# Optimization experiments

Hardware: AMD Instinct MI355X
Metric: run time of the kernel (lower is better)

The kernel has to match this reference:

```python
import jax, jax.numpy as jnp
import numpy as np

N = 50000
E = 800000
D = 128


def setup_inputs() -> dict:
    key = jax.random.key(0)
    ks = jax.random.split(key, 6)
    x = jax.random.normal(ks[0], (N, D), dtype=jnp.float32)
    edge_index = jax.random.randint(ks[1], (2, E), 0, N, dtype=jnp.int32)
    scale = 1.0 / np.sqrt(D)
    Ws = jax.random.uniform(ks[2], (D, D), jnp.float32, -scale, scale)
    bs = jax.random.uniform(ks[3], (D,), jnp.float32, -scale, scale)
    Wn = jax.random.uniform(ks[4], (D, D), jnp.float32, -scale, scale)
    bn = jax.random.uniform(ks[5], (D,), jnp.float32, -scale, scale)
    return {"x": x, "edge_index": edge_index, "Ws": Ws, "bs": bs, "Wn": Wn, "bn": bn}


def reference(x, edge_index, Ws, bs, Wn, bn):
    # x: [N, D]; edge_index: [2, E] with rows (src, dst)
    src = edge_index[0]
    dst = edge_index[1]
    n = x.shape[0]
    # scatter-sum of gathered source features onto destinations
    agg = jax.ops.segment_sum(x[src], dst, num_segments=n)  # [N, D]
    deg = jax.ops.segment_sum(jnp.ones(dst.shape, x.dtype), dst, num_segments=n)  # [N]
    neigh = agg / jnp.clip(deg, 1.0)[:, None]  # mean aggregation, clamp deg>=1
    # torch Linear: y = x @ W.T + b
    return jax.nn.relu(x @ Ws.T + bs + neigh @ Wn.T + bn)
```

## Files before the change

### kernel.cpp

```cpp
#include <hip/hip_runtime.h>

#define D 128
#define CAP 64

typedef short bf16x8 __attribute__((ext_vector_type(8)));
typedef float f32x4 __attribute__((ext_vector_type(4)));

__device__ __forceinline__ unsigned f2bf(float f) {
    unsigned u = __builtin_bit_cast(unsigned, f);
    return (u + 0x7FFFu + ((u >> 16) & 1u)) >> 16;
}
__device__ __forceinline__ float bflo(unsigned u) {
    return __builtin_bit_cast(float, u << 16);
}
__device__ __forceinline__ float bfhi(unsigned u) {
    return __builtin_bit_cast(float, u & 0xFFFF0000u);
}

__global__ __launch_bounds__(256)
void sage_prep(const float* __restrict__ x,
               const float* __restrict__ Ws,
               const float* __restrict__ Wn,
               const int* __restrict__ ei,
               unsigned short* __restrict__ xb,
               unsigned short* __restrict__ Wsb,
               unsigned short* __restrict__ Wnb,
               unsigned short* __restrict__ srcs,
               int* __restrict__ cnt,
               int nD4, int DD4, int convBlocks, int E)
{
    const int tid = threadIdx.x;
    if ((int)blockIdx.x < convBlocks) {
        int i4 = blockIdx.x * 256 + tid;
        const float* src; unsigned short* dst; int off;
        if (i4 < nD4)                { src = x;  dst = xb;  off = i4; }
        else if (i4 < nD4 + DD4)     { src = Ws; dst = Wsb; off = i4 - nD4; }
        else if (i4 < nD4 + 2 * DD4) { src = Wn; dst = Wnb; off = i4 - nD4 - DD4; }
        else return;
        float4 v = reinterpret_cast<const float4*>(src)[off];
        ushort4 o;
        o.x = (unsigned short)f2bf(v.x);
        o.y = (unsigned short)f2bf(v.y);
        o.z = (unsigned short)f2bf(v.z);
        o.w = (unsigned short)f2bf(v.w);
        reinterpret_cast<ushort4*>(dst)[off] = o;
    } else {
        int e = (blockIdx.x - convBlocks) * 256 + tid;
        if (e < E) {
            int src = ei[e];
            int dst = ei[E + e];
            int pos = atomicAdd(&cnt[dst], 1);
            if (pos < CAP) srcs[dst * CAP + pos] = (unsigned short)src;
        }
    }
}

__global__ void sage_gather(const unsigned* __restrict__ xb32,
                            const unsigned short* __restrict__ srcs,
                            const int* __restrict__ cnt,
                            unsigned* __restrict__ nb32, int n)
{
    int wid = __builtin_amdgcn_readfirstlane(
        blockIdx.x * (blockDim.x >> 6) + (threadIdx.x >> 6));
    if (wid >= n) return;
    int lane = threadIdx.x & 63;
    int c = cnt[wid];
    if (c > CAP) c = CAP;
    const unsigned short* b = srcs + (size_t)wid * CAP;
    float ax = 0.0f, ay = 0.0f;
    int i = 0;
    for (; i + 3 < c; i += 4) {
        int s0 = b[i + 0];
        int s1 = b[i + 1];
        int s2 = b[i + 2];
        int s3 = b[i + 3];
        unsigned u0 = xb32[(size_t)s0 * 64 + lane];
        unsigned u1 = xb32[(size_t)s1 * 64 + lane];
        unsigned u2 = xb32[(size_t)s2 * 64 + lane];
        unsigned u3 = xb32[(size_t)s3 * 64 + lane];
        ax += (bflo(u0) + bflo(u1)) + (bflo(u2) + bflo(u3));
        ay += (bfhi(u0) + bfhi(u1)) + (bfhi(u2) + bfhi(u3));
    }
    for (; i < c; ++i) {
        unsigned u0 = xb32[(size_t)b[i] * 64 + lane];
        ax += bflo(u0);
        ay += bfhi(u0);
    }
    float inv = 1.0f / fmaxf((float)c, 1.0f);
    nb32[(size_t)wid * 64 + lane] = f2bf(ax * inv) | (f2bf(ay * inv) << 16);
}

__global__ __launch_bounds__(256)
void sage_mfma(const unsigned short* __restrict__ xb,
               const unsigned short* __restrict__ nb,
               const unsigned short* __restrict__ Wsb,
               const unsigned short* __restrict__ Wnb,
               const float* __restrict__ bs,
               const float* __restrict__ bn,
               float* __restrict__ out, int n, int ntiles)
{
    int wave = (blockIdx.x * blockDim.x + threadIdx.x) >> 6;
    if (wave >= ntiles) return;
    int lane = threadIdx.x & 63;
    int r0 = wave * 16;
    int arow = r0 + (lane & 15);
    if (arow >= n) arow = n - 1;
    int kq = (lane >> 4) * 8;

    const unsigned short* xrow = xb + (size_t)arow * D + kq;
    const unsigned short* nrow = nb + (size_t)arow * D + kq;
    bf16x8 axf[4], anf[4];
#pragma unroll
    for (int ks = 0; ks < 4; ++ks) {
        axf[ks] = *reinterpret_cast<const bf16x8*>(xrow + ks * 32);
        anf[ks] = *reinterpret_cast<const bf16x8*>(nrow + ks * 32);
    }

    const int jl = lane & 15;
    const int outrow0 = r0 + (lane >> 4) * 4;
#pragma unroll
    for (int c = 0; c < 8; ++c) {
        int j = c * 16 + jl;
        const unsigned short* wsrow = Wsb + (size_t)j * D + kq;
        const unsigned short* wnrow = Wnb + (size_t)j * D + kq;
        f32x4 acc = {0.f, 0.f, 0.f, 0.f};
#pragma unroll
        for (int ks = 0; ks < 4; ++ks) {
            bf16x8 bsf = *reinterpret_cast<const bf16x8*>(wsrow + ks * 32);
            bf16x8 bnf = *reinterpret_cast<const bf16x8*>(wnrow + ks * 32);
            acc = __builtin_amdgcn_mfma_f32_16x16x32_bf16(axf[ks], bsf, acc, 0, 0, 0);
            acc = __builtin_amdgcn_mfma_f32_16x16x32_bf16(anf[ks], bnf, acc, 0, 0, 0);
        }
        float bias = bs[j] + bn[j];
#pragma unroll
        for (int r = 0; r < 4; ++r) {
            int row = outrow0 + r;
            if (row < n) {
                float v = acc[r] + bias;
                out[(size_t)row * D + j] = v > 0.f ? v : 0.f;
            }
        }
    }
}

extern "C" void kernel_launch(void* const* d_in, const int* in_sizes, int n_in,
                              void* d_out, int out_size, void* d_ws, size_t ws_size,
                              hipStream_t stream)
{
    const float* x  = (const float*)d_in[0];
    const int*   ei = (const int*)d_in[1];
    const float* Ws = (const float*)d_in[2];
    const float* bs = (const float*)d_in[3];
    const float* Wn = (const float*)d_in[4];
    const float* bn = (const float*)d_in[5];
    float* out = (float*)d_out;

    const int n = in_sizes[0] / D;
    const int E = in_sizes[1] / 2;

    unsigned short* xb   = (unsigned short*)d_ws;
    unsigned short* nb   = xb + (size_t)n * D;
    unsigned short* srcs = nb + (size_t)n * D;
    int*            cnt  = (int*)(srcs + (size_t)n * CAP);
    unsigned short* Wsb  = (unsigned short*)(cnt + n);
    unsigned short* Wnb  = Wsb + D * D;

    hipMemsetAsync(cnt, 0, (size_t)n * sizeof(int), stream);

    const int nD4 = n * D / 4;
    const int DD4 = D * D / 4;
    const int convBlocks   = (nD4 + 2 * DD4 + 255) / 256;
    const int bucketBlocks = (E + 255) / 256;

    sage_prep<<<convBlocks + bucketBlocks, 256, 0, stream>>>(
        x, Ws, Wn, ei, xb, Wsb, Wnb, srcs, cnt, nD4, DD4, convBlocks, E);

    {
        int wpb = 256 / 64;
        int blocks = (n + wpb - 1) / wpb;
        sage_gather<<<blocks, 256, 0, stream>>>((const unsigned*)xb, srcs, cnt,
                                                (unsigned*)nb, n);
    }

    {
        int ntiles = (n + 15) / 16;
        int blocks = (ntiles * 64 + 255) / 256;
        sage_mfma<<<blocks, 256, 0, stream>>>(xb, nb, Wsb, Wnb, bs, bn, out, n, ntiles);
    }
}
```

Baseline: 216.1 us.

## Fuse neighbor gather with MFMA projection via LDS, reorder prep blocks

Merges the gather/mean kernel and the MFMA linear kernel into one kernel. Each block of 4 waves aggregates 16 nodes into a swizzled LDS tile and then computes the 16x128 output, with each wave taking 32 output columns. This removes the global round-trip of the bf16 neighbor matrix and one kernel launch. The prep kernel now runs the edge-bucketing blocks before the conversion blocks and writes the bucket entries with nontemporal stores. In exchange, each block runs a gather phase and a compute phase separated by a barrier, which may reduce latency hiding, and each wave now loads only its own slice of the weights.

```diff
diff --git a/kernel.cpp b/kernel.cpp
--- a/kernel.cpp
+++ b/kernel.cpp
@@ -27,11 +27,21 @@
                unsigned short* __restrict__ Wnb,
                unsigned short* __restrict__ srcs,
                int* __restrict__ cnt,
-               int nD4, int DD4, int convBlocks, int E)
+               int nD4, int DD4, int bucketBlocks, int E)
 {
     const int tid = threadIdx.x;
-    if ((int)blockIdx.x < convBlocks) {
-        int i4 = blockIdx.x * 256 + tid;
+    if ((int)blockIdx.x < bucketBlocks) {
+        int e = blockIdx.x * 256 + tid;
+        if (e < E) {
+            int src = ei[e];
+            int dst = ei[E + e];
+            int pos = atomicAdd(&cnt[dst], 1);
+            if (pos < CAP)
+                __builtin_nontemporal_store((unsigned short)src,
+                                            &srcs[dst * CAP + pos]);
+        }
+    } else {
+        int i4 = (blockIdx.x - bucketBlocks) * 256 + tid;
         const float* src; unsigned short* dst; int off;
         if (i4 < nD4)                { src = x;  dst = xb;  off = i4; }
         else if (i4 < nD4 + DD4)     { src = Ws; dst = Wsb; off = i4 - nD4; }
@@ -44,87 +54,81 @@
         o.z = (unsigned short)f2bf(v.z);
         o.w = (unsigned short)f2bf(v.w);
         reinterpret_cast<ushort4*>(dst)[off] = o;
-    } else {
-        int e = (blockIdx.x - convBlocks) * 256 + tid;
-        if (e < E) {
-            int src = ei[e];
-            int dst = ei[E + e];
-            int pos = atomicAdd(&cnt[dst], 1);
-            if (pos < CAP) srcs[dst * CAP + pos] = (unsigned short)src;
-        }
     }
 }
 
-__global__ void sage_gather(const unsigned* __restrict__ xb32,
-                            const unsigned short* __restrict__ srcs,
-                            const int* __restrict__ cnt,
-                            unsigned* __restrict__ nb32, int n)
+__global__ __launch_bounds__(256)
+void sage_fused(const unsigned* __restrict__ xb32,
+                const unsigned short* __restrict__ xb,
+                const unsigned short* __restrict__ srcs,
+                const int* __restrict__ cnt,
+                const unsigned short* __restrict__ Wsb,
+                const unsigned short* __restrict__ Wnb,
+                const float* __restrict__ bs,
+                const float* __restrict__ bn,
+                float* __restrict__ out, int n)
 {
-    int wid = __builtin_amdgcn_readfirstlane(
-        blockIdx.x * (blockDim.x >> 6) + (threadIdx.x >> 6));
-    if (wid >= n) return;
-    int lane = threadIdx.x & 63;
-    int c = cnt[wid];
-    if (c > CAP) c = CAP;
-    const unsigned short* b = srcs + (size_t)wid * CAP;
-    float ax = 0.0f, ay = 0.0f;
-    int i = 0;
-    for (; i + 3 < c; i += 4) {
-        int s0 = b[i + 0];
-        int s1 = b[i + 1];
-        int s2 = b[i + 2];
-        int s3 = b[i + 3];
-        unsigned u0 = xb32[(size_t)s0 * 64 + lane];
-        unsigned u1 = xb32[(size_t)s1 * 64 + lane];
-        unsigned u2 = xb32[(size_t)s2 * 64 + lane];
-        unsigned u3 = xb32[(size_t)s3 * 64 + lane];
-        ax += (bflo(u0) + bflo(u1)) + (bflo(u2) + bflo(u3));
-        ay += (bfhi(u0) + bfhi(u1)) + (bfhi(u2) + bfhi(u3));
+    __shared__ unsigned nlds[16 * 64];
+    const int lane = threadIdx.x & 63;
+    const int w = threadIdx.x >> 6;
+    const int r0 = blockIdx.x * 16;
+
+    #pragma unroll
+    for (int i = 0; i < 4; ++i) {
+        const int nl = w * 4 + i;
+        const int node = __builtin_amdgcn_readfirstlane(r0 + nl);
+        float ax = 0.f, ay = 0.f;
+        int c = 0;
+        if (node < n) { c = cnt[node]; c = c > CAP ? CAP : c; }
+        const unsigned short* b = srcs + (size_t)node * CAP;
+        int k = 0;
+        for (; k + 3 < c; k += 4) {
+            int s0 = b[k + 0];
+            int s1 = b[k + 1];
+            int s2 = b[k + 2];
+            int s3 = b[k + 3];
+            unsigned u0 = xb32[(size_t)s0 * 64 + lane];
+            unsigned u1 = xb32[(size_t)s1 * 64 + lane];
+            unsigned u2 = xb32[(size_t)s2 * 64 + lane];
+            unsigned u3 = xb32[(size_t)s3 * 64 + lane];
+            ax += (bflo(u0) + bflo(u1)) + (bflo(u2) + bflo(u3));
+            ay += (bfhi(u0) + bfhi(u1)) + (bfhi(u2) + bfhi(u3));
+        }
+        for (; k < c; ++k) {
+            unsigned u = xb32[(size_t)b[k] * 64 + lane];
+            ax += bflo(u);
+            ay += bfhi(u);
+        }
+        float inv = 1.f / fmaxf((float)c, 1.f);
+        nlds[nl * 64 + (lane ^ ((nl & 7) << 2))] =
+            f2bf(ax * inv) | (f2bf(ay * inv) << 16);
     }
-    for (; i < c; ++i) {
-        unsigned u0 = xb32[(size_t)b[i] * 64 + lane];
-        ax += bflo(u0);
-        ay += bfhi(u0);
-    }
-    float inv = 1.0f / fmaxf((float)c, 1.0f);
-    nb32[(size_t)wid * 64 + lane] = f2bf(ax * inv) | (f2bf(ay * inv) << 16);
-}
+    __syncthreads();
 
-__global__ __launch_bounds__(256)
-void sage_mfma(const unsigned short* __restrict__ xb,
-               const unsigned short* __restrict__ nb,
-               const unsigned short* __restrict__ Wsb,
-               const unsigned short* __restrict__ Wnb,
-               const float* __restrict__ bs,
-               const float* __restrict__ bn,
-               float* __restrict__ out, int n, int ntiles)
-{
-    int wave = (blockIdx.x * blockDim.x + threadIdx.x) >> 6;
-    if (wave >= ntiles) return;
-    int lane = threadIdx.x & 63;
-    int r0 = wave * 16;
-    int arow = r0 + (lane & 15);
+    const int jl = lane & 15;
+    int arow = r0 + jl;
     if (arow >= n) arow = n - 1;
-    int kq = (lane >> 4) * 8;
+    const int kq = (lane >> 4) * 8;
 
     const unsigned short* xrow = xb + (size_t)arow * D + kq;
-    const unsigned short* nrow = nb + (size_t)arow * D + kq;
+    const char* lbase = (const char*)nlds + jl * 256;
+    const unsigned sw = (unsigned)((jl & 7) << 4);
     bf16x8 axf[4], anf[4];
-#pragma unroll
+    #pragma unroll
     for (int ks = 0; ks < 4; ++ks) {
         axf[ks] = *reinterpret_cast<const bf16x8*>(xrow + ks * 32);
-        anf[ks] = *reinterpret_cast<const bf16x8*>(nrow + ks * 32);
+        anf[ks] = *reinterpret_cast<const bf16x8*>(
+            lbase + (((unsigned)((kq << 1) + (ks << 6))) ^ sw));
     }
 
-    const int jl = lane & 15;
     const int outrow0 = r0 + (lane >> 4) * 4;
-#pragma unroll
-    for (int c = 0; c < 8; ++c) {
-        int j = c * 16 + jl;
+    #pragma unroll
+    for (int cc = 0; cc < 2; ++cc) {
+        const int j = (w * 2 + cc) * 16 + jl;
         const unsigned short* wsrow = Wsb + (size_t)j * D + kq;
         const unsigned short* wnrow = Wnb + (size_t)j * D + kq;
         f32x4 acc = {0.f, 0.f, 0.f, 0.f};
-#pragma unroll
+        #pragma unroll
         for (int ks = 0; ks < 4; ++ks) {
             bf16x8 bsf = *reinterpret_cast<const bf16x8*>(wsrow + ks * 32);
             bf16x8 bnf = *reinterpret_cast<const bf16x8*>(wnrow + ks * 32);
@@ -132,7 +136,7 @@
             acc = __builtin_amdgcn_mfma_f32_16x16x32_bf16(anf[ks], bnf, acc, 0, 0, 0);
         }
         float bias = bs[j] + bn[j];
-#pragma unroll
+        #pragma unroll
         for (int r = 0; r < 4; ++r) {
             int row = outrow0 + r;
             if (row < n) {
@@ -159,8 +163,7 @@
     const int E = in_sizes[1] / 2;
 
     unsigned short* xb   = (unsigned short*)d_ws;
-    unsigned short* nb   = xb + (size_t)n * D;
-    unsigned short* srcs = nb + (size_t)n * D;
+    unsigned short* srcs = xb + (size_t)n * D;
     int*            cnt  = (int*)(srcs + (size_t)n * CAP);
     unsigned short* Wsb  = (unsigned short*)(cnt + n);
     unsigned short* Wnb  = Wsb + D * D;
@@ -169,22 +172,15 @@
 
     const int nD4 = n * D / 4;
     const int DD4 = D * D / 4;
+    const int bucketBlocks = (E + 255) / 256;
     const int convBlocks   = (nD4 + 2 * DD4 + 255) / 256;
-    const int bucketBlocks = (E + 255) / 256;
 
-    sage_prep<<<convBlocks + bucketBlocks, 256, 0, stream>>>(
-        x, Ws, Wn, ei, xb, Wsb, Wnb, srcs, cnt, nD4, DD4, convBlocks, E);
+    sage_prep<<<bucketBlocks + convBlocks, 256, 0, stream>>>(
+        x, Ws, Wn, ei, xb, Wsb, Wnb, srcs, cnt, nD4, DD4, bucketBlocks, E);
 
     {
-        int wpb = 256 / 64;
-        int blocks = (n + wpb - 1) / wpb;
-        sage_gather<<<blocks, 256, 0, stream>>>((const unsigned*)xb, srcs, cnt,
-                                                (unsigned*)nb, n);
-    }
-
-    {
-        int ntiles = (n + 15) / 16;
-        int blocks = (ntiles * 64 + 255) / 256;
-        sage_mfma<<<blocks, 256, 0, stream>>>(xb, nb, Wsb, Wnb, bs, bn, out, n, ntiles);
+        int tiles = (n + 15) / 16;
+        sage_fused<<<tiles, 256, 0, stream>>>((const unsigned*)xb, xb, srcs, cnt,
+                                              Wsb, Wnb, bs, bn, out, n);
     }
 }
```

Measured after the change: 201.1 us. -6.9%, faster.
